# Kernel optimization log

Hardware: AMD Instinct MI355X
Metric: run time of the kernel (lower is better)

## Reference

```python
import jax, jax.numpy as jnp
import numpy as np

B, S, H = 128, 1024, 256
NEG = 1e9

def setup_inputs() -> dict:
    key = jax.random.key(0)
    ks = jax.random.split(key, 11)
    sc = 0.05
    return {
        'ref': jax.random.normal(ks[0], (B, S, H), jnp.float32),
        'query': jax.random.normal(ks[1], (B, H), jnp.float32),
        'mask': jax.random.randint(ks[2], (B, S), 0, 2, jnp.int32),
        'wg': jax.random.normal(ks[3], (H, H), jnp.float32) * sc,
        'bg': jax.random.normal(ks[4], (H,), jnp.float32) * sc,
        'wqg': jax.random.normal(ks[5], (H, H), jnp.float32) * sc,
        'vg': jax.random.normal(ks[6], (H,), jnp.float32) * sc,
        'wp': jax.random.normal(ks[7], (H, H), jnp.float32) * sc,
        'bp': jax.random.normal(ks[8], (H,), jnp.float32) * sc,
        'wqp': jax.random.normal(ks[9], (H, H), jnp.float32) * sc,
        'vp': jax.random.normal(ks[10], (H,), jnp.float32) * sc,
    }

def reference(ref, query, mask, wg, bg, wqg, vg, wp, bp, wqp, vp):
    # Bahdanau additive pointer attention with glimpse, per PointerDecoder.pointer_net
    maskf = mask.astype(ref.dtype)
    # glimpse attention
    enc_g = jnp.einsum('bsd,hd->bsh', ref, wg) + bg            # conv1d kernel=1
    q_g = jnp.einsum('bd,hd->bh', query, wqg)                   # w_q_g (no bias)
    scores_g = jnp.einsum('bsh,h->bs', jnp.tanh(enc_g + q_g[:, None, :]), vg)
    att_g = jax.nn.softmax(scores_g - maskf * NEG, axis=-1)     # [B,S]
    glimpse = jnp.einsum('bs,bsd->bd', att_g, ref) + query      # [B,H]
    # pointer scores
    enc_p = jnp.einsum('bsd,hd->bsh', ref, wp) + bp
    q_p = jnp.einsum('bd,hd->bh', glimpse, wqp)
    scores_p = jnp.einsum('bsh,h->bs', jnp.tanh(enc_p + q_p[:, None, :]), vp)
    masked_scores = scores_p - maskf * NEG                      # [B,S]
    return masked_scores
```

## Files before the change

kernel.cpp:

```cpp
#include <hip/hip_runtime.h>

#define Bb 128
#define Ss 1024
#define Hh 256
#define NEGF 1e9f

typedef short bf16x8 __attribute__((ext_vector_type(8)));
typedef float f32x4 __attribute__((ext_vector_type(4)));

__device__ __forceinline__ short f2bf(float f) {
    union { float f; unsigned u; } c; c.f = f;
    return (short)((c.u + 0x8000u) >> 16);
}

__device__ __forceinline__ float bfhi2f(unsigned u) {
    union { unsigned u; float f; } c; c.u = u & 0xFFFF0000u; return c.f;
}
__device__ __forceinline__ float bflo2f(unsigned u) {
    union { unsigned u; float f; } c; c.u = u << 16; return c.f;
}

__device__ __forceinline__ bf16x8 ld_bf8_f32(const float* p) {
    const float4* p4 = (const float4*)p;
    float4 a = p4[0], b = p4[1];
    bf16x8 r;
    r[0] = f2bf(a.x); r[1] = f2bf(a.y); r[2] = f2bf(a.z); r[3] = f2bf(a.w);
    r[4] = f2bf(b.x); r[5] = f2bf(b.y); r[6] = f2bf(b.z); r[7] = f2bf(b.w);
    return r;
}

__device__ __forceinline__ float fast_tanh(float x) {
    float cl = fminf(fmaxf(x, -10.f), 10.f);
    float e = __expf(2.f * cl);
    return (e - 1.f) * __builtin_amdgcn_rcpf(e + 1.f);
}

__device__ __forceinline__ void stage16(const short* g, short* l) {
    __builtin_amdgcn_global_load_lds((const __attribute__((address_space(1))) void*)g,
                                     (__attribute__((address_space(3))) void*)l, 16, 0, 0);
}

__global__ __launch_bounds__(256) void prep_kernel(const float* __restrict__ wg,
                                                   const float* __restrict__ wp,
                                                   const float* __restrict__ query,
                                                   const float* __restrict__ wqg,
                                                   const float* __restrict__ bg,
                                                   short* __restrict__ wgb,
                                                   short* __restrict__ wpb,
                                                   float* __restrict__ qbias_g) {
    int blk = blockIdx.x, t = threadIdx.x;
    if (blk < 256) {
        int i = blk * 256 + t;
        wgb[i] = f2bf(wg[i]);
        wpb[i] = f2bf(wp[i]);
    } else {
        int b = blk - 256;
        const float4* qr = (const float4*)(query + b * Hh);
        const float4* wr = (const float4*)(wqg + t * Hh);
        float acc = 0.f;
#pragma unroll 8
        for (int i = 0; i < Hh / 4; ++i) {
            float4 q4 = qr[i], w4 = wr[i];
            acc += q4.x * w4.x + q4.y * w4.y + q4.z * w4.z + q4.w * w4.w;
        }
        qbias_g[b * Hh + t] = acc + bg[t];
    }
}

template <int MASKED, int LOADF32>
__global__ __launch_bounds__(256) void scores_mfma(const float* __restrict__ reff,
                                                   const short* __restrict__ refb_in,
                                                   short* __restrict__ refb_out,
                                                   const short* __restrict__ Wbf,
                                                   const float* __restrict__ qbias,
                                                   const float* __restrict__ vvec,
                                                   const int* __restrict__ mask,
                                                   float* __restrict__ out) {
    __shared__ short Wlds[2][8192];
    const int b = blockIdx.x;
    const int s0 = blockIdx.y * 128;
    const int t = threadIdx.x;
    const int wave = t >> 6;
    const int lane = t & 63;
    const int nl = lane & 15;
    const int quad = lane >> 4;
    const int rowbase = s0 + wave * 32;

    const int soff0 = (t & 15) * Hh + (t >> 6) * 32 + ((t >> 4) & 3) * 8;
    const int soff1 = soff0 + 128;
    const int dbase0 = wave * 512;
    const int dbase1 = 2048 + wave * 512;

    bf16x8 afrag[2][8];
#pragma unroll
    for (int rt = 0; rt < 2; ++rt) {
        const size_t rowoff = ((size_t)b * Ss + rowbase + rt * 16 + nl) * Hh;
        if (LOADF32) {
            const float* rp = reff + rowoff;
#pragma unroll
            for (int kb = 0; kb < 8; ++kb)
                afrag[rt][kb] = ld_bf8_f32(rp + kb * 32 + quad * 8);
            short* dst = refb_out + rowoff;
#pragma unroll
            for (int kb = 0; kb < 8; ++kb)
                *(bf16x8*)(dst + kb * 32 + quad * 8) = afrag[rt][kb];
        } else {
            const short* rp = refb_in + rowoff;
#pragma unroll
            for (int kb = 0; kb < 8; ++kb)
                afrag[rt][kb] = *(const bf16x8*)(rp + kb * 32 + quad * 8);
        }
    }

    stage16(Wbf + soff0, &Wlds[0][dbase0]);
    stage16(Wbf + soff1, &Wlds[0][dbase1]);
    stage16(Wbf + 16 * Hh + soff0, &Wlds[0][4096 + dbase0]);
    stage16(Wbf + 16 * Hh + soff1, &Wlds[0][4096 + dbase1]);
    __syncthreads();

    float sc[2][4] = {{0.f, 0.f, 0.f, 0.f}, {0.f, 0.f, 0.f, 0.f}};

    for (int nc2 = 0; nc2 < 8; ++nc2) {
        const int cur = nc2 & 1;
        if (nc2 < 7) {
            const short* g = Wbf + (size_t)(nc2 + 1) * 32 * Hh;
            stage16(g + soff0, &Wlds[1 - cur][dbase0]);
            stage16(g + soff1, &Wlds[1 - cur][dbase1]);
            stage16(g + 16 * Hh + soff0, &Wlds[1 - cur][4096 + dbase0]);
            stage16(g + 16 * Hh + soff1, &Wlds[1 - cur][4096 + dbase1]);
        }
#pragma unroll
        for (int h = 0; h < 2; ++h) {
            const int n = nc2 * 32 + h * 16 + nl;
            const float qb = qbias[b * Hh + n];
            const float vv = vvec[n];
            bf16x8 bfrag[8];
#pragma unroll
            for (int kb = 0; kb < 8; ++kb)
                bfrag[kb] = *(const bf16x8*)&Wlds[cur][h * 4096 + kb * 512 + lane * 8];
#pragma unroll
            for (int rt = 0; rt < 2; ++rt) {
                f32x4 c = {0.f, 0.f, 0.f, 0.f};
#pragma unroll
                for (int kb = 0; kb < 8; ++kb)
                    c = __builtin_amdgcn_mfma_f32_16x16x32_bf16(afrag[rt][kb], bfrag[kb], c, 0, 0, 0);
#pragma unroll
                for (int r = 0; r < 4; ++r)
                    sc[rt][r] += fast_tanh(c[r] + qb) * vv;
            }
        }
        __syncthreads();
    }

#pragma unroll
    for (int rt = 0; rt < 2; ++rt)
#pragma unroll
        for (int r = 0; r < 4; ++r) {
            float v = sc[rt][r];
            v += __shfl_xor(v, 1, 64);
            v += __shfl_xor(v, 2, 64);
            v += __shfl_xor(v, 4, 64);
            v += __shfl_xor(v, 8, 64);
            sc[rt][r] = v;
        }

    if (nl == 0) {
#pragma unroll
        for (int rt = 0; rt < 2; ++rt)
#pragma unroll
            for (int r = 0; r < 4; ++r) {
                int m = rowbase + rt * 16 + quad * 4 + r;
                float v = sc[rt][r];
                if (MASKED) v -= (float)mask[b * Ss + m] * NEGF;
                out[(size_t)b * Ss + m] = v;
            }
    }
}

__global__ __launch_bounds__(1024) void softmax_kernel(const float* __restrict__ scores,
                                                       const int* __restrict__ mask,
                                                       float* __restrict__ att) {
    int b = blockIdx.x, t = threadIdx.x;
    __shared__ float red[16];
    int idx = b * Ss + t;
    float x = scores[idx] - (float)mask[idx] * NEGF;

    float m = x;
#pragma unroll
    for (int o = 1; o < 64; o <<= 1) m = fmaxf(m, __shfl_xor(m, o, 64));
    if ((t & 63) == 0) red[t >> 6] = m;
    __syncthreads();
    float M = red[0];
#pragma unroll
    for (int j = 1; j < 16; ++j) M = fmaxf(M, red[j]);
    __syncthreads();

    float e = __expf(x - M);
    float s = e;
#pragma unroll
    for (int o = 1; o < 64; o <<= 1) s += __shfl_xor(s, o, 64);
    if ((t & 63) == 0) red[t >> 6] = s;
    __syncthreads();
    float S = 0.f;
#pragma unroll
    for (int j = 0; j < 16; ++j) S += red[j];

    att[idx] = e * __builtin_amdgcn_rcpf(S);
}

__global__ __launch_bounds__(256) void glimpse_part(const unsigned* __restrict__ refb,
                                                    const float* __restrict__ att,
                                                    float* __restrict__ gpart) {
    int b = blockIdx.x, q = blockIdx.y, t = threadIdx.x;
    const int c = t & 31;
    const int rg = t >> 5;
    __shared__ float part[8][Hh];
    const unsigned* base = refb + ((size_t)(b * Ss + q * 128)) * (Hh / 2);
    const float* ap = att + b * Ss + q * 128;

    float acc[8] = {0.f, 0.f, 0.f, 0.f, 0.f, 0.f, 0.f, 0.f};
#pragma unroll 4
    for (int it = 0; it < 16; ++it) {
        int row = it * 8 + rg;
        float a = ap[row];
        uint4 v = *(const uint4*)(base + (size_t)row * (Hh / 2) + c * 4);
        acc[0] += a * bflo2f(v.x); acc[1] += a * bfhi2f(v.x);
        acc[2] += a * bflo2f(v.y); acc[3] += a * bfhi2f(v.y);
        acc[4] += a * bflo2f(v.z); acc[5] += a * bfhi2f(v.z);
        acc[6] += a * bflo2f(v.w); acc[7] += a * bfhi2f(v.w);
    }
#pragma unroll
    for (int j = 0; j < 8; ++j) part[rg][c * 8 + j] = acc[j];
    __syncthreads();
    float s = 0.f;
#pragma unroll
    for (int g = 0; g < 8; ++g) s += part[g][t];
    gpart[(size_t)(b * 8 + q) * Hh + t] = s;
}

__global__ __launch_bounds__(256) void qbias_p_kernel(const float* __restrict__ gpart,
                                                      const float* __restrict__ query,
                                                      const float* __restrict__ wqp,
                                                      const float* __restrict__ bp,
                                                      float* __restrict__ out) {
    int b = blockIdx.x, t = threadIdx.x;
    __shared__ __align__(16) float gl[Hh];
    float g = query[b * Hh + t];
#pragma unroll
    for (int q = 0; q < 8; ++q) g += gpart[(b * 8 + q) * Hh + t];
    gl[t] = g;
    __syncthreads();
    const float4* wr = (const float4*)(wqp + t * Hh);
    const float4* gp = (const float4*)gl;
    float acc = 0.f;
#pragma unroll 8
    for (int i = 0; i < Hh / 4; ++i) {
        float4 w4 = wr[i];
        float4 g4 = gp[i];
        acc += w4.x * g4.x + w4.y * g4.y + w4.z * g4.z + w4.w * g4.w;
    }
    out[b * Hh + t] = acc + bp[t];
}

extern "C" void kernel_launch(void* const* d_in, const int* in_sizes, int n_in,
                              void* d_out, int out_size, void* d_ws, size_t ws_size,
                              hipStream_t stream) {
    const float* ref   = (const float*)d_in[0];
    const float* query = (const float*)d_in[1];
    const int*   mask  = (const int*)d_in[2];
    const float* wg    = (const float*)d_in[3];
    const float* bg    = (const float*)d_in[4];
    const float* wqg   = (const float*)d_in[5];
    const float* vg    = (const float*)d_in[6];
    const float* wp    = (const float*)d_in[7];
    const float* bp    = (const float*)d_in[8];
    const float* wqp   = (const float*)d_in[9];
    const float* vp    = (const float*)d_in[10];
    float* out = (float*)d_out;

    char* ws = (char*)d_ws;
    short* ref_bf   = (short*)(ws + 0);
    size_t off = (size_t)Bb * Ss * Hh * 2;
    short* wg_bf    = (short*)(ws + off);               off += 131072;
    short* wp_bf    = (short*)(ws + off);               off += 131072;
    float* qbias_g  = (float*)(ws + off);               off += 131072;
    float* qbias_p  = (float*)(ws + off);               off += 131072;
    float* scores_g = (float*)(ws + off);               off += 524288;
    float* att      = (float*)(ws + off);               off += 524288;
    float* gpart    = (float*)(ws + off);

    prep_kernel<<<384, 256, 0, stream>>>(wg, wp, query, wqg, bg, wg_bf, wp_bf, qbias_g);
    scores_mfma<0, 1><<<dim3(Bb, Ss / 128), 256, 0, stream>>>(
        ref, nullptr, ref_bf, wg_bf, qbias_g, vg, nullptr, scores_g);
    softmax_kernel<<<Bb, Ss, 0, stream>>>(scores_g, mask, att);
    glimpse_part<<<dim3(Bb, 8), 256, 0, stream>>>((const unsigned*)ref_bf, att, gpart);
    qbias_p_kernel<<<Bb, Hh, 0, stream>>>(gpart, query, wqp, bp, qbias_p);
    scores_mfma<1, 0><<<dim3(Bb, Ss / 128), 256, 0, stream>>>(
        nullptr, ref_bf, nullptr, wp_bf, qbias_p, vp, mask, out);
}
```

Measured before the change: 297.3 us.

## Stage full bf16 weight matrix in LDS once per 1024-thread block

The scores kernel now uses 1024-thread blocks that load the entire 256x256 bf16 weight matrix (128 KB) into LDS once, then each wave handles a 32-row tile across all 16 output column chunks without further barriers. This replaces the old 256-thread blocks that double-buffered 32-column weight slices with a barrier per step and reloaded the weights for every 128-row block. The goal is to cut redundant weight traffic and synchronisation. The cost is that the large LDS footprint limits residency to one block per CU, so there is less latency hiding for the ref loads, and the grid shrinks to 256 blocks.

```diff
diff --git a/kernel.cpp b/kernel.cpp
--- a/kernel.cpp
+++ b/kernel.cpp
@@ -68,112 +68,93 @@
 }
 
 template <int MASKED, int LOADF32>
-__global__ __launch_bounds__(256) void scores_mfma(const float* __restrict__ reff,
-                                                   const short* __restrict__ refb_in,
-                                                   short* __restrict__ refb_out,
-                                                   const short* __restrict__ Wbf,
-                                                   const float* __restrict__ qbias,
-                                                   const float* __restrict__ vvec,
-                                                   const int* __restrict__ mask,
-                                                   float* __restrict__ out) {
-    __shared__ short Wlds[2][8192];
-    const int b = blockIdx.x;
-    const int s0 = blockIdx.y * 128;
+__global__ __launch_bounds__(1024) void scores_mfma(const float* __restrict__ reff,
+                                                    const short* __restrict__ refb_in,
+                                                    short* __restrict__ refb_out,
+                                                    const short* __restrict__ Wbf,
+                                                    const float* __restrict__ qbias,
+                                                    const float* __restrict__ vvec,
+                                                    const int* __restrict__ mask,
+                                                    float* __restrict__ out) {
+    __shared__ __align__(16) short Wlds[65536];
     const int t = threadIdx.x;
     const int wave = t >> 6;
     const int lane = t & 63;
     const int nl = lane & 15;
     const int quad = lane >> 4;
-    const int rowbase = s0 + wave * 32;
-
-    const int soff0 = (t & 15) * Hh + (t >> 6) * 32 + ((t >> 4) & 3) * 8;
-    const int soff1 = soff0 + 128;
-    const int dbase0 = wave * 512;
-    const int dbase1 = 2048 + wave * 512;
-
-    bf16x8 afrag[2][8];
+
+    {
+        const short* g = Wbf + (wave * 16 + nl) * Hh + quad * 8;
+        short* l = &Wlds[wave * 4096];
+#pragma unroll
+        for (int kb = 0; kb < 8; ++kb)
+            stage16(g + kb * 32, l + kb * 512);
+    }
+
+    const int tile = blockIdx.x * 16 + wave;
+    const int b = tile >> 5;
+    const int srow0 = (tile & 31) * 32;
+    const float* qb_row = qbias + b * Hh;
+
+    __syncthreads();
+
 #pragma unroll
     for (int rt = 0; rt < 2; ++rt) {
-        const size_t rowoff = ((size_t)b * Ss + rowbase + rt * 16 + nl) * Hh;
+        const size_t rowoff = ((size_t)b * Ss + srow0 + rt * 16 + nl) * Hh;
+
+        bf16x8 afrag[8];
         if (LOADF32) {
-            const float* rp = reff + rowoff;
-#pragma unroll
-            for (int kb = 0; kb < 8; ++kb)
-                afrag[rt][kb] = ld_bf8_f32(rp + kb * 32 + quad * 8);
-            short* dst = refb_out + rowoff;
-#pragma unroll
-            for (int kb = 0; kb < 8; ++kb)
-                *(bf16x8*)(dst + kb * 32 + quad * 8) = afrag[rt][kb];
+            const float* rp = reff + rowoff + quad * 8;
+#pragma unroll
+            for (int kb = 0; kb < 8; ++kb)
+                afrag[kb] = ld_bf8_f32(rp + kb * 32);
+            short* dst = refb_out + rowoff + quad * 8;
+#pragma unroll
+            for (int kb = 0; kb < 8; ++kb)
+                *(bf16x8*)(dst + kb * 32) = afrag[kb];
         } else {
-            const short* rp = refb_in + rowoff;
-#pragma unroll
-            for (int kb = 0; kb < 8; ++kb)
-                afrag[rt][kb] = *(const bf16x8*)(rp + kb * 32 + quad * 8);
-        }
-    }
-
-    stage16(Wbf + soff0, &Wlds[0][dbase0]);
-    stage16(Wbf + soff1, &Wlds[0][dbase1]);
-    stage16(Wbf + 16 * Hh + soff0, &Wlds[0][4096 + dbase0]);
-    stage16(Wbf + 16 * Hh + soff1, &Wlds[0][4096 + dbase1]);
-    __syncthreads();
-
-    float sc[2][4] = {{0.f, 0.f, 0.f, 0.f}, {0.f, 0.f, 0.f, 0.f}};
-
-    for (int nc2 = 0; nc2 < 8; ++nc2) {
-        const int cur = nc2 & 1;
-        if (nc2 < 7) {
-            const short* g = Wbf + (size_t)(nc2 + 1) * 32 * Hh;
-            stage16(g + soff0, &Wlds[1 - cur][dbase0]);
-            stage16(g + soff1, &Wlds[1 - cur][dbase1]);
-            stage16(g + 16 * Hh + soff0, &Wlds[1 - cur][4096 + dbase0]);
-            stage16(g + 16 * Hh + soff1, &Wlds[1 - cur][4096 + dbase1]);
-        }
-#pragma unroll
-        for (int h = 0; h < 2; ++h) {
-            const int n = nc2 * 32 + h * 16 + nl;
-            const float qb = qbias[b * Hh + n];
+            const short* rp = refb_in + rowoff + quad * 8;
+#pragma unroll
+            for (int kb = 0; kb < 8; ++kb)
+                afrag[kb] = *(const bf16x8*)(rp + kb * 32);
+        }
+
+        float sc[4] = {0.f, 0.f, 0.f, 0.f};
+#pragma unroll
+        for (int nc = 0; nc < 16; ++nc) {
+            const int n = nc * 16 + nl;
+            const float qb = qb_row[n];
             const float vv = vvec[n];
-            bf16x8 bfrag[8];
-#pragma unroll
-            for (int kb = 0; kb < 8; ++kb)
-                bfrag[kb] = *(const bf16x8*)&Wlds[cur][h * 4096 + kb * 512 + lane * 8];
-#pragma unroll
-            for (int rt = 0; rt < 2; ++rt) {
-                f32x4 c = {0.f, 0.f, 0.f, 0.f};
-#pragma unroll
-                for (int kb = 0; kb < 8; ++kb)
-                    c = __builtin_amdgcn_mfma_f32_16x16x32_bf16(afrag[rt][kb], bfrag[kb], c, 0, 0, 0);
-#pragma unroll
-                for (int r = 0; r < 4; ++r)
-                    sc[rt][r] += fast_tanh(c[r] + qb) * vv;
-            }
-        }
-        __syncthreads();
-    }
-
-#pragma unroll
-    for (int rt = 0; rt < 2; ++rt)
+            const short* wl = &Wlds[nc * 4096 + lane * 8];
+            f32x4 c = {0.f, 0.f, 0.f, 0.f};
+#pragma unroll
+            for (int kb = 0; kb < 8; ++kb)
+                c = __builtin_amdgcn_mfma_f32_16x16x32_bf16(
+                    afrag[kb], *(const bf16x8*)(wl + kb * 512), c, 0, 0, 0);
+#pragma unroll
+            for (int r = 0; r < 4; ++r)
+                sc[r] += fast_tanh(c[r] + qb) * vv;
+        }
+
 #pragma unroll
         for (int r = 0; r < 4; ++r) {
-            float v = sc[rt][r];
+            float v = sc[r];
             v += __shfl_xor(v, 1, 64);
             v += __shfl_xor(v, 2, 64);
             v += __shfl_xor(v, 4, 64);
             v += __shfl_xor(v, 8, 64);
-            sc[rt][r] = v;
-        }
-
-    if (nl == 0) {
-#pragma unroll
-        for (int rt = 0; rt < 2; ++rt)
+            sc[r] = v;
+        }
+
+        if (nl == 0) {
 #pragma unroll
             for (int r = 0; r < 4; ++r) {
-                int m = rowbase + rt * 16 + quad * 4 + r;
-                float v = sc[rt][r];
+                int m = srow0 + rt * 16 + quad * 4 + r;
+                float v = sc[r];
                 if (MASKED) v -= (float)mask[b * Ss + m] * NEGF;
                 out[(size_t)b * Ss + m] = v;
             }
+        }
     }
 }
 
@@ -290,11 +271,11 @@
     float* gpart    = (float*)(ws + off);
 
     prep_kernel<<<384, 256, 0, stream>>>(wg, wp, query, wqg, bg, wg_bf, wp_bf, qbias_g);
-    scores_mfma<0, 1><<<dim3(Bb, Ss / 128), 256, 0, stream>>>(
+    scores_mfma<0, 1><<<256, 1024, 0, stream>>>(
         ref, nullptr, ref_bf, wg_bf, qbias_g, vg, nullptr, scores_g);
     softmax_kernel<<<Bb, Ss, 0, stream>>>(scores_g, mask, att);
     glimpse_part<<<dim3(Bb, 8), 256, 0, stream>>>((const unsigned*)ref_bf, att, gpart);
     qbias_p_kernel<<<Bb, Hh, 0, stream>>>(gpart, query, wqp, bp, qbias_p);
-    scores_mfma<1, 0><<<dim3(Bb, Ss / 128), 256, 0, stream>>>(
+    scores_mfma<1, 0><<<256, 1024, 0, stream>>>(
         nullptr, ref_bf, nullptr, wp_bf, qbias_p, vp, mask, out);
 }
```

Result: slower. 321.6 us (+8.2%).
